# Kernel optimization log

Measured on AMD Instinct MI355X. Metric: run time of the kernel, lower is better.

The kernel has to match this reference:

```python
import jax, jax.numpy as jnp
import numpy as np

N, D, H, C, E = 16384, 768, 768, 2, 20

def setup_inputs() -> dict:
    key = jax.random.key(0)
    k1, k2, k3, k4, k5, k6 = jax.random.split(key, 6)
    return {
        "embeddings": jax.random.normal(k1, (N, D), dtype=jnp.float32),
        "component_idx": jax.random.randint(k2, (N,), 0, E, dtype=jnp.int64),
        "W1": jax.random.normal(k3, (E, D, H), dtype=jnp.float32) * (1.0 / np.sqrt(D)),
        "b1": jnp.zeros((E, H), dtype=jnp.float32),
        "W2": jax.random.normal(k4, (E, H, C), dtype=jnp.float32) * (1.0 / np.sqrt(H)),
        "b2": jnp.zeros((E, C), dtype=jnp.float32),
    }

def reference(embeddings, component_idx, W1, b1, W2, b2):
    # Each token n goes through expert component_idx[n]:
    #   y = relu(x @ W1[e] + b1[e]) @ W2[e] + b2[e]
    # The torch module's mask/cat/argsort reassembly is mathematically a
    # per-token select of its own expert's output at the original position.
    # Dense-expert formulation (standard jax MoE fallback), then gather.
    h = jax.nn.relu(jnp.einsum('nd,edh->enh', embeddings, W1) + b1[:, None, :])  # [E,N,H]
    y = jnp.einsum('enh,ehc->enc', h, W2) + b2[:, None, :]                        # [E,N,C]
    n_idx = jnp.arange(embeddings.shape[0])
    return y[component_idx, n_idx]  # [N,C]
```

## Files before the change

kernel.cpp:

```cpp
#include <hip/hip_runtime.h>

#define N_D 768
#define N_H 768
#define N_C 2
#define N_E 20
#define MT 128
#define NT 128
#define BK 32

typedef __attribute__((ext_vector_type(8))) short short8;
typedef __attribute__((ext_vector_type(4))) float f32x4;

__device__ __forceinline__ unsigned short f2bf(float f) {
  unsigned u = __builtin_bit_cast(unsigned, f);
  u += 0x7FFFu + ((u >> 16) & 1u);
  return (unsigned short)(u >> 16);
}
__device__ __forceinline__ float bf2f(unsigned short s) {
  unsigned u = ((unsigned)s) << 16;
  return __builtin_bit_cast(float, u);
}

#define GLD_LDS16(gp, lp)                                                        \
  __builtin_amdgcn_global_load_lds(                                              \
      (const __attribute__((address_space(1))) void*)(gp),                       \
      (__attribute__((address_space(3))) void*)(lp), 16, 0, 0)


__global__ __launch_bounds__(256) void k_hist(const int* __restrict__ cidx,
                                              int* __restrict__ counts, int n) {
  __shared__ int lc[N_E];
  if (threadIdx.x < N_E) lc[threadIdx.x] = 0;
  __syncthreads();
  for (int i = blockIdx.x * blockDim.x + threadIdx.x; i < n;
       i += gridDim.x * blockDim.x) {
    int e = cidx[i];
    e = e < 0 ? 0 : (e >= N_E ? N_E - 1 : e);
    atomicAdd(&lc[e], 1);
  }
  __syncthreads();
  if (threadIdx.x < N_E) atomicAdd(&counts[threadIdx.x], lc[threadIdx.x]);
}

__global__ void k_scan(const int* __restrict__ counts, int* __restrict__ offsets,
                       int* __restrict__ cursor) {
  if (threadIdx.x == 0) {
    int run = 0;
    for (int e = 0; e < N_E; ++e) {
      offsets[e] = run;
      cursor[e] = run;
      run += counts[e];
    }
  }
}

__global__ __launch_bounds__(256) void k_scatter(const int* __restrict__ cidx,
                                                 int* __restrict__ cursor,
                                                 int* __restrict__ sorted, int n) {
  __shared__ int lc[N_E];
  __shared__ int lbase[N_E];
  int tid = threadIdx.x;
  if (tid < N_E) lc[tid] = 0;
  __syncthreads();
  int i = blockIdx.x * blockDim.x + tid;
  int e = 0, p = 0;
  if (i < n) {
    e = cidx[i];
    e = e < 0 ? 0 : (e >= N_E ? N_E - 1 : e);
    p = atomicAdd(&lc[e], 1);
  }
  __syncthreads();
  if (tid < N_E) lbase[tid] = atomicAdd(&cursor[tid], lc[tid]);
  __syncthreads();
  if (i < n) sorted[lbase[e] + p] = i;
}


__global__ __launch_bounds__(256) void k_w1_cvt(const float* __restrict__ W1,
                                                unsigned short* __restrict__ W1t) {
  __shared__ float tile[32][33];
  int e = blockIdx.z;
  int h0 = blockIdx.x * 32, d0 = blockIdx.y * 32;
  const float* src = W1 + (size_t)e * N_D * N_H;
  unsigned short* dst = W1t + (size_t)e * N_H * N_D;
  int tx = threadIdx.x & 31, ty = threadIdx.x >> 5;
  for (int s = 0; s < 4; ++s)
    tile[ty + 8 * s][tx] = src[(size_t)(d0 + ty + 8 * s) * N_H + h0 + tx];
  __syncthreads();
  for (int s = 0; s < 4; ++s)
    dst[(size_t)(h0 + ty + 8 * s) * N_D + d0 + tx] = f2bf(tile[tx][ty + 8 * s]);
}


__global__ __launch_bounds__(256, 2) void k_gemm1(
    const float* __restrict__ emb, const float* __restrict__ b1,
    const unsigned short* __restrict__ W1t, const int* __restrict__ sorted,
    const int* __restrict__ counts, const int* __restrict__ offsets,
    unsigned short* __restrict__ hbuf) {
  const int e = blockIdx.z;
  const int cnt = counts[e];
  const int m0 = blockIdx.y * MT;
  if (m0 >= cnt) return;
  const int off = offsets[e];
  const int n0 = blockIdx.x * NT;

  __shared__ unsigned short lA[MT * BK];
  __shared__ unsigned short lB[NT * BK];
  __shared__ int lRow[MT];

  const int tid = threadIdx.x;
  if (tid < MT) {
    int m = m0 + tid;
    lRow[tid] = sorted[off + (m < cnt ? m : 0)];
  }
  __syncthreads();

  const int wid = tid >> 6, lane = tid & 63;
  const int wm = (wid >> 1) * 64, wn = (wid & 1) * 64;
  const int quad = lane >> 4, lm = lane & 15;

  const float4* aptr[4];
  int arow[4], akq[4];
  for (int s = 0; s < 4; ++s) {
    int g = tid + s * 256;
    arow[s] = g >> 3;
    akq[s] = g & 7;
    aptr[s] = (const float4*)(emb + (size_t)lRow[arow[s]] * N_D) + akq[s];
  }

  const unsigned short* Bbase = W1t + (size_t)e * N_H * N_D + (size_t)n0 * N_D;
  const unsigned short* bgp[2];
  unsigned short* blp[2];
  for (int t = 0; t < 2; ++t) {
    int r = (wid * 2 + t) * 16 + (lane >> 2);
    bgp[t] = Bbase + (size_t)r * N_D + (lane & 3) * 8;
    blp[t] = &lB[(wid * 2 + t) * 16 * BK];
  }

  f32x4 acc[4][4] = {};

  for (int kt = 0; kt < N_D / BK; ++kt) {
    __syncthreads();
    GLD_LDS16(bgp[0] + kt * BK, blp[0]);
    GLD_LDS16(bgp[1] + kt * BK, blp[1]);
    for (int s = 0; s < 4; ++s) {
      float4 v = aptr[s][kt * (BK / 4)];
      ushort4 b4;
      b4.x = f2bf(v.x);
      b4.y = f2bf(v.y);
      b4.z = f2bf(v.z);
      b4.w = f2bf(v.w);
      *(ushort4*)&lA[arow[s] * BK + akq[s] * 4] = b4;
    }
    __syncthreads();

    short8 af[4], bfr[4];
    for (int i = 0; i < 4; ++i)
      af[i] = *(const short8*)&lA[(wm + i * 16 + lm) * BK + quad * 8];
    for (int j = 0; j < 4; ++j)
      bfr[j] = *(const short8*)&lB[(wn + j * 16 + lm) * BK + quad * 8];
    for (int i = 0; i < 4; ++i)
      for (int j = 0; j < 4; ++j)
        acc[i][j] =
            __builtin_amdgcn_mfma_f32_16x16x32_bf16(af[i], bfr[j], acc[i][j], 0, 0, 0);
  }

  const int cnt_rel = cnt - m0;
  for (int j = 0; j < 4; ++j) {
    int col = n0 + wn + j * 16 + lm;
    float bias = b1[e * N_H + col];
    for (int i = 0; i < 4; ++i) {
      int rbase = wm + i * 16 + quad * 4;
      f32x4 a = acc[i][j];
      for (int r = 0; r < 4; ++r) {
        int mrel = rbase + r;
        if (mrel < cnt_rel) {
          float h = a[r] + bias;
          h = h > 0.f ? h : 0.f;
          hbuf[(size_t)(off + m0 + mrel) * N_H + col] = f2bf(h);
        }
      }
    }
  }
}


__global__ __launch_bounds__(256) void k_layer2(
    const unsigned short* __restrict__ hbuf, const int* __restrict__ sorted,
    const int* __restrict__ cidx, const float* __restrict__ W2,
    const float* __restrict__ b2, float* __restrict__ out, int n) {
  int p = blockIdx.x * 4 + (threadIdx.x >> 6);
  if (p >= n) return;
  int lane = threadIdx.x & 63;
  int token = sorted[p];
  int e = cidx[token];
  e = e < 0 ? 0 : (e >= N_E ? N_E - 1 : e);
  const unsigned short* hrow = hbuf + (size_t)p * N_H;
  const float* w2e = W2 + (size_t)e * N_H * N_C;
  float a0 = 0.f, a1 = 0.f;
  for (int it = 0; it < N_H / 128; ++it) {
    int col = it * 128 + lane * 2;
    unsigned v = *(const unsigned*)&hrow[col];
    float h0 = bf2f((unsigned short)(v & 0xFFFFu));
    float h1 = bf2f((unsigned short)(v >> 16));
    float4 w = *(const float4*)&w2e[col * 2];
    a0 += h0 * w.x + h1 * w.z;
    a1 += h0 * w.y + h1 * w.w;
  }
  for (int s = 32; s >= 1; s >>= 1) {
    a0 += __shfl_xor(a0, s, 64);
    a1 += __shfl_xor(a1, s, 64);
  }
  if (lane == 0) {
    out[(size_t)token * N_C + 0] = a0 + b2[e * N_C + 0];
    out[(size_t)token * N_C + 1] = a1 + b2[e * N_C + 1];
  }
}


extern "C" void kernel_launch(void* const* d_in, const int* in_sizes, int n_in,
                              void* d_out, int out_size, void* d_ws, size_t ws_size,
                              hipStream_t stream) {
  const float* emb = (const float*)d_in[0];
  const int* cidx = (const int*)d_in[1];
  const float* W1 = (const float*)d_in[2];
  const float* b1 = (const float*)d_in[3];
  const float* W2 = (const float*)d_in[4];
  const float* b2 = (const float*)d_in[5];
  float* out = (float*)d_out;
  const int n = in_sizes[1];

  char* ws = (char*)d_ws;
  int* counts = (int*)ws;
  int* offsets = (int*)(ws + 256);
  int* cursor = (int*)(ws + 512);
  int* sorted = (int*)(ws + 1024);
  size_t sorted_bytes = ((size_t)n * 4 + 1023) & ~(size_t)1023;
  unsigned short* W1t = (unsigned short*)(ws + 1024 + sorted_bytes);
  unsigned short* hbuf =
      (unsigned short*)((char*)W1t + (size_t)N_E * N_D * N_H * 2);

  hipMemsetAsync(d_ws, 0, 1024, stream);
  int nb = (n + 255) / 256;
  k_hist<<<nb, 256, 0, stream>>>(cidx, counts, n);
  k_scan<<<1, 64, 0, stream>>>(counts, offsets, cursor);
  k_scatter<<<nb, 256, 0, stream>>>(cidx, cursor, sorted, n);
  k_w1_cvt<<<dim3(N_H / 32, N_D / 32, N_E), 256, 0, stream>>>(W1, W1t);
  k_gemm1<<<dim3(N_H / NT, (n + MT - 1) / MT, N_E), 256, 0, stream>>>(
      emb, b1, W1t, sorted, counts, offsets, hbuf);
  k_layer2<<<(n + 3) / 4, 256, 0, stream>>>(hbuf, sorted, cidx, W2, b2, out, n);
}
```

Baseline: 243.2 us.

## Fuse layer-2 into GEMM epilogue, pre-gather bf16 activations, compact tile list

Adds a gather kernel that writes expert-sorted embeddings as bf16, so the GEMM loads both operands with direct global-to-LDS loads. The second layer is fused into the GEMM epilogue, with partial dot products combined by shuffles and atomic adds into a zeroed output, which removes the hidden buffer round trip and the separate layer-2 kernel. The GEMM grid now walks a compact list of non-empty tiles instead of a sparse expert-by-row grid, and the weight transpose uses wider 64x64 tiles with vector accesses. In exchange there is an extra gather pass, float atomics that make summation order nondeterministic, and a fixed cap of 160 tiles that could drop work if the token distribution is skewed.

Result: faster. 224.0 us (-7.9%).

```diff
diff --git a/kernel.cpp b/kernel.cpp
--- a/kernel.cpp
+++ b/kernel.cpp
@@ -7,6 +7,7 @@
 #define MT 128
 #define NT 128
 #define BK 32
+#define MAX_TILES 160
 
 typedef __attribute__((ext_vector_type(8))) short short8;
 typedef __attribute__((ext_vector_type(4))) float f32x4;
@@ -15,10 +16,6 @@
   unsigned u = __builtin_bit_cast(unsigned, f);
   u += 0x7FFFu + ((u >> 16) & 1u);
   return (unsigned short)(u >> 16);
-}
-__device__ __forceinline__ float bf2f(unsigned short s) {
-  unsigned u = ((unsigned)s) << 16;
-  return __builtin_bit_cast(float, u);
 }
 
 #define GLD_LDS16(gp, lp)                                                        \
@@ -43,14 +40,18 @@
 }
 
 __global__ void k_scan(const int* __restrict__ counts, int* __restrict__ offsets,
-                       int* __restrict__ cursor) {
+                       int* __restrict__ cursor, int* __restrict__ tiles,
+                       int* __restrict__ numTiles) {
   if (threadIdx.x == 0) {
-    int run = 0;
+    int run = 0, t = 0;
     for (int e = 0; e < N_E; ++e) {
       offsets[e] = run;
       cursor[e] = run;
+      int nt = (counts[e] + MT - 1) / MT;
+      for (int m = 0; m < nt && t < MAX_TILES; ++m) tiles[t++] = (e << 8) | m;
       run += counts[e];
     }
+    *numTiles = t;
   }
 }
 
@@ -76,82 +77,93 @@
 }
 
 
+__global__ __launch_bounds__(192) void k_gather(const float* __restrict__ emb,
+                                                const int* __restrict__ sorted,
+                                                unsigned short* __restrict__ Xg,
+                                                int n) {
+  int row = blockIdx.x;
+  int j = threadIdx.x;
+  ushort4 o;
+  if (row < n) {
+    float4 v = ((const float4*)(emb + (size_t)sorted[row] * N_D))[j];
+    o.x = f2bf(v.x);
+    o.y = f2bf(v.y);
+    o.z = f2bf(v.z);
+    o.w = f2bf(v.w);
+  } else {
+    o.x = o.y = o.z = o.w = 0;
+  }
+  ((ushort4*)(Xg + (size_t)row * N_D))[j] = o;
+}
+
+
 __global__ __launch_bounds__(256) void k_w1_cvt(const float* __restrict__ W1,
                                                 unsigned short* __restrict__ W1t) {
-  __shared__ float tile[32][33];
-  int e = blockIdx.z;
-  int h0 = blockIdx.x * 32, d0 = blockIdx.y * 32;
+  __shared__ float tile[64][65];
+  int e = blockIdx.z, h0 = blockIdx.x * 64, d0 = blockIdx.y * 64;
   const float* src = W1 + (size_t)e * N_D * N_H;
   unsigned short* dst = W1t + (size_t)e * N_H * N_D;
-  int tx = threadIdx.x & 31, ty = threadIdx.x >> 5;
-  for (int s = 0; s < 4; ++s)
-    tile[ty + 8 * s][tx] = src[(size_t)(d0 + ty + 8 * s) * N_H + h0 + tx];
-  __syncthreads();
-  for (int s = 0; s < 4; ++s)
-    dst[(size_t)(h0 + ty + 8 * s) * N_D + d0 + tx] = f2bf(tile[tx][ty + 8 * s]);
-}
-
-
-__global__ __launch_bounds__(256, 2) void k_gemm1(
-    const float* __restrict__ emb, const float* __restrict__ b1,
-    const unsigned short* __restrict__ W1t, const int* __restrict__ sorted,
+  int tx = threadIdx.x & 15, ty = threadIdx.x >> 4;
+  for (int s = 0; s < 4; ++s) {
+    int d = s * 16 + ty;
+    float4 v = *(const float4*)&src[(size_t)(d0 + d) * N_H + h0 + tx * 4];
+    tile[d][tx * 4 + 0] = v.x;
+    tile[d][tx * 4 + 1] = v.y;
+    tile[d][tx * 4 + 2] = v.z;
+    tile[d][tx * 4 + 3] = v.w;
+  }
+  __syncthreads();
+  for (int s = 0; s < 4; ++s) {
+    int h = s * 16 + ty;
+    ushort4 o;
+    o.x = f2bf(tile[tx * 4 + 0][h]);
+    o.y = f2bf(tile[tx * 4 + 1][h]);
+    o.z = f2bf(tile[tx * 4 + 2][h]);
+    o.w = f2bf(tile[tx * 4 + 3][h]);
+    *(ushort4*)&dst[(size_t)(h0 + h) * N_D + d0 + tx * 4] = o;
+  }
+}
+
+
+__global__ __launch_bounds__(256, 2) void k_gemm(
+    const unsigned short* __restrict__ Xg, const unsigned short* __restrict__ W1t,
+    const float* __restrict__ b1, const float* __restrict__ W2,
+    const float* __restrict__ b2, const int* __restrict__ sorted,
     const int* __restrict__ counts, const int* __restrict__ offsets,
-    unsigned short* __restrict__ hbuf) {
-  const int e = blockIdx.z;
-  const int cnt = counts[e];
-  const int m0 = blockIdx.y * MT;
-  if (m0 >= cnt) return;
+    const int* __restrict__ tiles, const int* __restrict__ numTiles,
+    float* __restrict__ out) {
+  if ((int)blockIdx.y >= *numTiles) return;
+  const int tv = tiles[blockIdx.y];
+  const int e = tv >> 8;
+  const int m0 = (tv & 255) * MT;
   const int off = offsets[e];
+  const int cnt_rel = counts[e] - m0;
   const int n0 = blockIdx.x * NT;
 
   __shared__ unsigned short lA[MT * BK];
   __shared__ unsigned short lB[NT * BK];
-  __shared__ int lRow[MT];
 
   const int tid = threadIdx.x;
-  if (tid < MT) {
-    int m = m0 + tid;
-    lRow[tid] = sorted[off + (m < cnt ? m : 0)];
-  }
-  __syncthreads();
-
   const int wid = tid >> 6, lane = tid & 63;
   const int wm = (wid >> 1) * 64, wn = (wid & 1) * 64;
   const int quad = lane >> 4, lm = lane & 15;
 
-  const float4* aptr[4];
-  int arow[4], akq[4];
-  for (int s = 0; s < 4; ++s) {
-    int g = tid + s * 256;
-    arow[s] = g >> 3;
-    akq[s] = g & 7;
-    aptr[s] = (const float4*)(emb + (size_t)lRow[arow[s]] * N_D) + akq[s];
-  }
-
-  const unsigned short* Bbase = W1t + (size_t)e * N_H * N_D + (size_t)n0 * N_D;
-  const unsigned short* bgp[2];
-  unsigned short* blp[2];
-  for (int t = 0; t < 2; ++t) {
-    int r = (wid * 2 + t) * 16 + (lane >> 2);
-    bgp[t] = Bbase + (size_t)r * N_D + (lane & 3) * 8;
-    blp[t] = &lB[(wid * 2 + t) * 16 * BK];
-  }
+  const unsigned short* ag =
+      Xg + (size_t)(off + m0 + wid * 32 + (lane >> 2)) * N_D + (lane & 3) * 8;
+  const unsigned short* bg = W1t + (size_t)e * N_H * N_D +
+                             (size_t)(n0 + wid * 32 + (lane >> 2)) * N_D +
+                             (lane & 3) * 8;
 
   f32x4 acc[4][4] = {};
 
   for (int kt = 0; kt < N_D / BK; ++kt) {
     __syncthreads();
-    GLD_LDS16(bgp[0] + kt * BK, blp[0]);
-    GLD_LDS16(bgp[1] + kt * BK, blp[1]);
-    for (int s = 0; s < 4; ++s) {
-      float4 v = aptr[s][kt * (BK / 4)];
-      ushort4 b4;
-      b4.x = f2bf(v.x);
-      b4.y = f2bf(v.y);
-      b4.z = f2bf(v.z);
-      b4.w = f2bf(v.w);
-      *(ushort4*)&lA[arow[s] * BK + akq[s] * 4] = b4;
-    }
+    const unsigned short* agk = ag + kt * BK;
+    const unsigned short* bgk = bg + kt * BK;
+    GLD_LDS16(agk, &lA[(wid * 32) * BK]);
+    GLD_LDS16(agk + 16 * N_D, &lA[(wid * 32 + 16) * BK]);
+    GLD_LDS16(bgk, &lB[(wid * 32) * BK]);
+    GLD_LDS16(bgk + 16 * N_D, &lB[(wid * 32 + 16) * BK]);
     __syncthreads();
 
     short8 af[4], bfr[4];
@@ -165,55 +177,45 @@
             __builtin_amdgcn_mfma_f32_16x16x32_bf16(af[i], bfr[j], acc[i][j], 0, 0, 0);
   }
 
-  const int cnt_rel = cnt - m0;
+  float y0[4][4], y1[4][4];
+  for (int i = 0; i < 4; ++i)
+    for (int r = 0; r < 4; ++r) y0[i][r] = y1[i][r] = 0.f;
+
   for (int j = 0; j < 4; ++j) {
     int col = n0 + wn + j * 16 + lm;
     float bias = b1[e * N_H + col];
+    float2 w2 = *(const float2*)&W2[((size_t)e * N_H + col) * N_C];
     for (int i = 0; i < 4; ++i) {
-      int rbase = wm + i * 16 + quad * 4;
       f32x4 a = acc[i][j];
       for (int r = 0; r < 4; ++r) {
-        int mrel = rbase + r;
+        float h = a[r] + bias;
+        h = h > 0.f ? h : 0.f;
+        y0[i][r] += h * w2.x;
+        y1[i][r] += h * w2.y;
+      }
+    }
+  }
+  for (int s = 1; s < 16; s <<= 1) {
+    for (int i = 0; i < 4; ++i)
+      for (int r = 0; r < 4; ++r) {
+        y0[i][r] += __shfl_xor(y0[i][r], s, 64);
+        y1[i][r] += __shfl_xor(y1[i][r], s, 64);
+      }
+  }
+  if (lm == 0) {
+    const bool add_bias = (n0 == 0) && (wn == 0);
+    float bb0 = add_bias ? b2[e * N_C + 0] : 0.f;
+    float bb1 = add_bias ? b2[e * N_C + 1] : 0.f;
+    for (int i = 0; i < 4; ++i) {
+      for (int r = 0; r < 4; ++r) {
+        int mrel = wm + i * 16 + quad * 4 + r;
         if (mrel < cnt_rel) {
-          float h = a[r] + bias;
-          h = h > 0.f ? h : 0.f;
-          hbuf[(size_t)(off + m0 + mrel) * N_H + col] = f2bf(h);
+          int token = sorted[off + m0 + mrel];
+          atomicAdd(&out[(size_t)token * N_C + 0], y0[i][r] + bb0);
+          atomicAdd(&out[(size_t)token * N_C + 1], y1[i][r] + bb1);
         }
       }
     }
-  }
-}
-
-
-__global__ __launch_bounds__(256) void k_layer2(
-    const unsigned short* __restrict__ hbuf, const int* __restrict__ sorted,
-    const int* __restrict__ cidx, const float* __restrict__ W2,
-    const float* __restrict__ b2, float* __restrict__ out, int n) {
-  int p = blockIdx.x * 4 + (threadIdx.x >> 6);
-  if (p >= n) return;
-  int lane = threadIdx.x & 63;
-  int token = sorted[p];
-  int e = cidx[token];
-  e = e < 0 ? 0 : (e >= N_E ? N_E - 1 : e);
-  const unsigned short* hrow = hbuf + (size_t)p * N_H;
-  const float* w2e = W2 + (size_t)e * N_H * N_C;
-  float a0 = 0.f, a1 = 0.f;
-  for (int it = 0; it < N_H / 128; ++it) {
-    int col = it * 128 + lane * 2;
-    unsigned v = *(const unsigned*)&hrow[col];
-    float h0 = bf2f((unsigned short)(v & 0xFFFFu));
-    float h1 = bf2f((unsigned short)(v >> 16));
-    float4 w = *(const float4*)&w2e[col * 2];
-    a0 += h0 * w.x + h1 * w.z;
-    a1 += h0 * w.y + h1 * w.w;
-  }
-  for (int s = 32; s >= 1; s >>= 1) {
-    a0 += __shfl_xor(a0, s, 64);
-    a1 += __shfl_xor(a1, s, 64);
-  }
-  if (lane == 0) {
-    out[(size_t)token * N_C + 0] = a0 + b2[e * N_C + 0];
-    out[(size_t)token * N_C + 1] = a1 + b2[e * N_C + 1];
   }
 }
 
@@ -232,21 +234,24 @@
 
   char* ws = (char*)d_ws;
   int* counts = (int*)ws;
-  int* offsets = (int*)(ws + 256);
-  int* cursor = (int*)(ws + 512);
-  int* sorted = (int*)(ws + 1024);
-  size_t sorted_bytes = ((size_t)n * 4 + 1023) & ~(size_t)1023;
-  unsigned short* W1t = (unsigned short*)(ws + 1024 + sorted_bytes);
-  unsigned short* hbuf =
-      (unsigned short*)((char*)W1t + (size_t)N_E * N_D * N_H * 2);
-
-  hipMemsetAsync(d_ws, 0, 1024, stream);
+  int* offsets = (int*)(ws + 128);
+  int* cursor = (int*)(ws + 256);
+  int* numTiles = (int*)(ws + 384);
+  int* tiles = (int*)(ws + 512);
+  int* sorted = (int*)(ws + 2048);
+  size_t sorted_bytes = ((size_t)n * 4 + 255) & ~(size_t)255;
+  unsigned short* Xg = (unsigned short*)(ws + 2048 + sorted_bytes);
+  int pcap = n + MT;
+  unsigned short* W1t = Xg + (size_t)pcap * N_D;
+
+  hipMemsetAsync(d_ws, 0, 2048, stream);
+  hipMemsetAsync(d_out, 0, (size_t)out_size * sizeof(float), stream);
   int nb = (n + 255) / 256;
   k_hist<<<nb, 256, 0, stream>>>(cidx, counts, n);
-  k_scan<<<1, 64, 0, stream>>>(counts, offsets, cursor);
+  k_scan<<<1, 64, 0, stream>>>(counts, offsets, cursor, tiles, numTiles);
   k_scatter<<<nb, 256, 0, stream>>>(cidx, cursor, sorted, n);
-  k_w1_cvt<<<dim3(N_H / 32, N_D / 32, N_E), 256, 0, stream>>>(W1, W1t);
-  k_gemm1<<<dim3(N_H / NT, (n + MT - 1) / MT, N_E), 256, 0, stream>>>(
-      emb, b1, W1t, sorted, counts, offsets, hbuf);
-  k_layer2<<<(n + 3) / 4, 256, 0, stream>>>(hbuf, sorted, cidx, W2, b2, out, n);
-}
+  k_gather<<<pcap, 192, 0, stream>>>(emb, sorted, Xg, n);
+  k_w1_cvt<<<dim3(N_H / 64, N_D / 64, N_E), 256, 0, stream>>>(W1, W1t);
+  k_gemm<<<dim3(N_H / NT, MAX_TILES), 256, 0, stream>>>(
+      Xg, W1t, b1, W2, b2, sorted, counts, offsets, tiles, numTiles, out);
+}
```
